# Performance work log

Measured on AMD Instinct MI355X. Metric: run time of the kernel, lower is better.

Reference implementation:

```python
import jax, jax.numpy as jnp
import numpy as np

# Contact model constants (from ContactModel defaults / hardcoded values)
STIFFNESS = 100000.0
DISSIPATION = 0.2
STATIC_FRICTION = 0.8
DYNAMIC_FRICTION = 0.8
VISCOUS_FRICTION = 0.5
TRANSITION_VELOCITY = 0.2
GROUND_HEIGHT = 0.0
DT = 0.05
RADIUS = 0.032
EPS = 1e-5
EPS2 = 1e-16
BV = 50.0
BD = 300.0

# 12 spheres: 6 right (bodies 4,5), 6 left (bodies 9,10)
SPHERE_BODY = np.array([4, 4, 4, 4, 5, 5, 9, 9, 9, 9, 10, 10], dtype=np.int32)
SPHERE_LOCAL = np.array([
    [0.00190115788407966, -0.01, -0.00382630379623308],
    [0.148386399942063,   -0.01, -0.028713422052654],
    [0.133001170607051,   -0.01,  0.0516362473449566],
    [0.0662346661991635,  -0.01,  0.0263641606741698],
    [0.06,                -0.01, -0.0187603084619177],
    [0.045,               -0.01,  0.0618569567549652],
    [0.00190115788407966, -0.01,  0.00382630379623308],
    [0.148386399942063,   -0.01,  0.028713422052654],
    [0.133001170607051,   -0.01, -0.0516362473449566],
    [0.0662346661991635,  -0.01, -0.0263641606741698],
    [0.06,                -0.01,  0.0187603084619177],
    [0.045,               -0.01, -0.0618569567549652],
], dtype=np.float32)
NORMAL = np.array([0.0, 1.0, 0.0], dtype=np.float32)


def _sphere_positions(joints, joints_ori):
    # joints: (B,24,3), joints_ori: (B,24,3,3) -> (B,12,3)
    body_pos = joints[:, SPHERE_BODY]            # (B,12,3)
    body_ori = joints_ori[:, SPHERE_BODY]        # (B,12,3,3)
    local = jnp.asarray(SPHERE_LOCAL)
    return body_pos + jnp.einsum('bsij,sj->bsi', body_ori, local)


def _contact_forces(pos, vel):
    # pos, vel: (B,S,3) -> forces (B,S,3); fully vectorized over spheres
    n = jnp.asarray(NORMAL)
    indentation = GROUND_HEIGHT - pos[..., 1]                    # (B,S)
    vnormal = vel[..., 1]                                        # dot(vel, [0,1,0])
    vtangent = vel - vnormal[..., None] * n                      # (B,S,3)
    ind_vel = -vnormal
    k = 0.5 * STIFFNESS ** (2.0 / 3.0)
    # sqrt(ind^2+eps)**1.5 == (ind^2+eps)**0.75
    fH = (4.0 / 3.0) * k * np.sqrt(RADIUS * k) * (indentation * indentation + EPS) ** 0.75
    fHd = fH * (1.0 + 1.5 * DISSIPATION * ind_vel)
    fn = ((0.5 * jnp.tanh(BV * (ind_vel + 1.0 / (1.5 * DISSIPATION))) + 0.5 + EPS2)
          * (0.5 * jnp.tanh(BD * indentation) + 0.5 + EPS2) * fHd)
    vslip = jnp.sqrt(jnp.sum(vtangent * vtangent, axis=-1) + EPS)
    vrel = vslip / TRANSITION_VELOCITY
    ffriction = fn * (jnp.minimum(vrel, 1.0)
                      * (DYNAMIC_FRICTION + 2.0 * (STATIC_FRICTION - DYNAMIC_FRICTION) / (1.0 + vrel * vrel))
                      + VISCOUS_FRICTION * vslip)
    force = fn[..., None] * n
    friction_force = ffriction[..., None] * (-vtangent) / (vslip[..., None] + EPS)
    return force + friction_force


def _cop_and_torque(pos, forces):
    # pos, forces: (B,S,3) -> cop (B,3), torque (B,3); vectorized batch version of the per-b loop
    vf = forces[..., 1]                          # (B,S)
    valid = vf > 0.0
    w = jnp.where(valid, vf, 0.0)
    tw = jnp.sum(w, axis=-1)                     # (B,)
    has = tw > 0.0
    tw_safe = jnp.where(has, tw, 1.0)
    cop_x = jnp.where(has, jnp.sum(pos[..., 0] * w, axis=-1) / tw_safe, 0.0)
    cop_y = jnp.where(has, GROUND_HEIGHT, 0.0)
    cop_z = jnp.where(has, jnp.sum(pos[..., 2] * w, axis=-1) / tw_safe, 0.0)
    cop = jnp.stack([cop_x, cop_y, cop_z], axis=-1)  # (B,3)
    r = pos - cop[:, None, :]
    f_masked = jnp.where(valid[..., None], forces, 0.0)  # only valid contacts contribute torque
    torque = jnp.sum(jnp.cross(r, f_masked), axis=1)
    return cop, torque


def setup_inputs() -> dict:
    key = jax.random.key(0)
    k1, k2 = jax.random.split(key)
    B = 262144
    joints = jax.random.normal(k1, (B, 24, 3), dtype=jnp.float32)
    joints_ori = jax.random.normal(k2, (B, 24, 3, 3), dtype=jnp.float32)
    return {"joints": joints, "joints_ori": joints_ori}


def reference(joints, joints_ori):
    pos = _sphere_positions(joints, joints_ori)              # (B,12,3)
    # finite-difference sphere velocity over frames (dt); zero at first frame
    vel = (pos - jnp.concatenate([pos[:1], pos[:-1]], axis=0)) / DT
    sphere_forces = _contact_forces(pos, vel)                # (B,12,3)

    force = jnp.sum(sphere_forces, axis=1)
    force_right = jnp.sum(sphere_forces[:, :6], axis=1)
    force_left = jnp.sum(sphere_forces[:, 6:], axis=1)
    cop, torque = _cop_and_torque(pos, sphere_forces)
    cop_right, torque_right = _cop_and_torque(pos[:, :6], sphere_forces[:, :6])
    cop_left, torque_left = _cop_and_torque(pos[:, 6:], sphere_forces[:, 6:])
    return (force, torque, cop, sphere_forces, pos,
            force_right, force_left, torque_right, torque_left, cop_right, cop_left)
```

## Files before the change

### kernel.cpp

```cpp
#include <hip/hip_runtime.h>
#include <math.h>


__device__ __constant__ float c_local[12][3] = {
    {0.00190115788407966f, -0.01f, -0.00382630379623308f},
    {0.148386399942063f,   -0.01f, -0.028713422052654f},
    {0.133001170607051f,   -0.01f,  0.0516362473449566f},
    {0.0662346661991635f,  -0.01f,  0.0263641606741698f},
    {0.06f,                -0.01f, -0.0187603084619177f},
    {0.045f,               -0.01f,  0.0618569567549652f},
    {0.00190115788407966f, -0.01f,  0.00382630379623308f},
    {0.148386399942063f,   -0.01f,  0.028713422052654f},
    {0.133001170607051f,   -0.01f, -0.0516362473449566f},
    {0.0662346661991635f,  -0.01f, -0.0263641606741698f},
    {0.06f,                -0.01f,  0.0187603084619177f},
    {0.045f,               -0.01f, -0.0618569567549652f}};

__global__ __launch_bounds__(256)
void contact_kernel(const float* __restrict__ joints,
                    const float* __restrict__ jori,
                    float* __restrict__ out, const int B)
{
    __shared__ float sbuf[256 * 37];
    const int tid = threadIdx.x;
    const int b = blockIdx.x * blockDim.x + tid;
    const bool full = ((B & 255) == 0);
    if (b >= B) return;

    float px[12], py[12], pz[12];
    float fx[12], fy[12], fz[12];

    {
        const int bodies[4] = {4, 5, 9, 10};
        const int sbeg[4]   = {0, 4, 6, 10};
        const int scnt[4]   = {4, 2, 4, 2};
        const int bp = (b > 0) ? (b - 1) : b;
        const float* jr  = joints + (size_t)b  * 72;
        const float* jrp = joints + (size_t)bp * 72;
        const float* mr  = jori   + (size_t)b  * 216;
        const float* mrp = jori   + (size_t)bp * 216;

        #pragma unroll
        for (int bi = 0; bi < 4; ++bi) {
            const int body = bodies[bi];
            const float jx = jr[body*3+0], jy = jr[body*3+1], jz = jr[body*3+2];
            const float* m = mr + body*9;
            const float m00=m[0],m01=m[1],m02=m[2];
            const float m10=m[3],m11=m[4],m12=m[5];
            const float m20=m[6],m21=m[7],m22=m[8];
            const float kx = jrp[body*3+0], ky = jrp[body*3+1], kz = jrp[body*3+2];
            const float* nn = mrp + body*9;
            const float n00=nn[0],n01=nn[1],n02=nn[2];
            const float n10=nn[3],n11=nn[4],n12=nn[5];
            const float n20=nn[6],n21=nn[7],n22=nn[8];
            #pragma unroll
            for (int si = 0; si < 4; ++si) {
                if (si < scnt[bi]) {
                    const int s = sbeg[bi] + si;
                    const float lx = c_local[s][0];
                    const float ly = c_local[s][1];
                    const float lz = c_local[s][2];
                    const float ax = jx + m00*lx + m01*ly + m02*lz;
                    const float ay = jy + m10*lx + m11*ly + m12*lz;
                    const float az = jz + m20*lx + m21*ly + m22*lz;
                    const float bx = kx + n00*lx + n01*ly + n02*lz;
                    const float by = ky + n10*lx + n11*ly + n12*lz;
                    const float bz = kz + n20*lx + n21*ly + n22*lz;
                    px[s] = ax; py[s] = ay; pz[s] = az;
                    fx[s] = (ax - bx) * 20.0f;
                    fy[s] = (ay - by) * 20.0f;
                    fz[s] = (az - bz) * 20.0f;
                }
            }
        }
    }

    const float KF  = 1077.21734501594f;
    const float CFH = (4.0f/3.0f) * KF * sqrtf(0.032f * KF);
    #pragma unroll
    for (int s = 0; s < 12; ++s) {
        const float vx = fx[s], vy = fy[s], vz = fz[s];
        const float ind     = -py[s];
        const float ind_vel = -vy;
        const float q   = ind*ind + 1e-5f;
        const float fH  = CFH * sqrtf(q * sqrtf(q));
        const float fHd = fH * (1.0f + 0.3f * ind_vel);
        const float t1 = (0.5f*tanhf(50.0f*(ind_vel + 3.3333333333333335f)) + 0.5f) + 1e-16f;
        const float t2 = (0.5f*tanhf(300.0f*ind) + 0.5f) + 1e-16f;
        const float fn = t1 * t2 * fHd;
        const float vslip = sqrtf(vx*vx + vz*vz + 1e-5f);
        const float vrel  = vslip * 5.0f;
        const float mu  = fminf(vrel, 1.0f) * 0.8f + 0.5f * vslip;
        const float ffr = fn * mu;
        const float sc  = ffr / (vslip + 1e-5f);
        fx[s] = -sc * vx;
        fy[s] = fn;
        fz[s] = -sc * vz;
    }

    float res[3][9];
    const int gs0[3] = {0, 0, 6};
    const int gs1[3] = {12, 6, 12};
    #pragma unroll
    for (int g = 0; g < 3; ++g) {
        float Fx=0.f, Fy=0.f, Fz=0.f, tw=0.f, sx=0.f, sz=0.f;
        #pragma unroll
        for (int s = 0; s < 12; ++s) {
            if (s >= gs0[g] && s < gs1[g]) {
                Fx += fx[s]; Fy += fy[s]; Fz += fz[s];
                const float w = fy[s] > 0.f ? fy[s] : 0.f;
                tw += w;
                sx += px[s] * w;
                sz += pz[s] * w;
            }
        }
        const bool has = tw > 0.f;
        const float cx = has ? sx / tw : 0.f;
        const float cz = has ? sz / tw : 0.f;
        float Tx=0.f, Ty=0.f, Tz=0.f;
        #pragma unroll
        for (int s = 0; s < 12; ++s) {
            if (s >= gs0[g] && s < gs1[g]) {
                if (fy[s] > 0.f) {
                    const float rx = px[s]-cx, ry = py[s], rz = pz[s]-cz;
                    Tx += ry*fz[s] - rz*fy[s];
                    Ty += rz*fx[s] - rx*fz[s];
                    Tz += rx*fy[s] - ry*fx[s];
                }
            }
        }
        res[g][0]=Fx; res[g][1]=Fy; res[g][2]=Fz;
        res[g][3]=Tx; res[g][4]=Ty; res[g][5]=Tz;
        res[g][6]=cx; res[g][7]=0.f; res[g][8]=cz;
    }

    const size_t sB = (size_t)B;
    const size_t t3 = (size_t)b * 3;
    float* o;
    o = out;           o[t3]=res[0][0]; o[t3+1]=res[0][1]; o[t3+2]=res[0][2];
    o = out + sB*3;    o[t3]=res[0][3]; o[t3+1]=res[0][4]; o[t3+2]=res[0][5];
    o = out + sB*6;    o[t3]=res[0][6]; o[t3+1]=res[0][7]; o[t3+2]=res[0][8];
    o = out + sB*81;   o[t3]=res[1][0]; o[t3+1]=res[1][1]; o[t3+2]=res[1][2];
    o = out + sB*84;   o[t3]=res[2][0]; o[t3+1]=res[2][1]; o[t3+2]=res[2][2];
    o = out + sB*87;   o[t3]=res[1][3]; o[t3+1]=res[1][4]; o[t3+2]=res[1][5];
    o = out + sB*90;   o[t3]=res[2][3]; o[t3+1]=res[2][4]; o[t3+2]=res[2][5];
    o = out + sB*93;   o[t3]=res[1][6]; o[t3+1]=res[1][7]; o[t3+2]=res[1][8];
    o = out + sB*96;   o[t3]=res[2][6]; o[t3+1]=res[2][7]; o[t3+2]=res[2][8];

    if (full) {
        #pragma unroll
        for (int s = 0; s < 12; ++s) {
            sbuf[tid*37 + s*3+0] = fx[s];
            sbuf[tid*37 + s*3+1] = fy[s];
            sbuf[tid*37 + s*3+2] = fz[s];
        }
        __syncthreads();
        {
            float4* dst = reinterpret_cast<float4*>(out + sB*9) + (size_t)blockIdx.x*2304;
            #pragma unroll
            for (int i = 0; i < 9; ++i) {
                const int j = tid + 256*i;
                const int g = 4*j;
                float v[4];
                #pragma unroll
                for (int e = 0; e < 4; ++e) {
                    const int gg = g+e; const int r = gg/36; const int c = gg-r*36;
                    v[e] = sbuf[r*37+c];
                }
                dst[j] = make_float4(v[0],v[1],v[2],v[3]);
            }
        }
        __syncthreads();
        #pragma unroll
        for (int s = 0; s < 12; ++s) {
            sbuf[tid*37 + s*3+0] = px[s];
            sbuf[tid*37 + s*3+1] = py[s];
            sbuf[tid*37 + s*3+2] = pz[s];
        }
        __syncthreads();
        {
            float4* dst = reinterpret_cast<float4*>(out + sB*45) + (size_t)blockIdx.x*2304;
            #pragma unroll
            for (int i = 0; i < 9; ++i) {
                const int j = tid + 256*i;
                const int g = 4*j;
                float v[4];
                #pragma unroll
                for (int e = 0; e < 4; ++e) {
                    const int gg = g+e; const int r = gg/36; const int c = gg-r*36;
                    v[e] = sbuf[r*37+c];
                }
                dst[j] = make_float4(v[0],v[1],v[2],v[3]);
            }
        }
    } else {
        float* osf = out + sB*9  + (size_t)b*36;
        float* opp = out + sB*45 + (size_t)b*36;
        #pragma unroll
        for (int s = 0; s < 12; ++s) {
            osf[s*3+0]=fx[s]; osf[s*3+1]=fy[s]; osf[s*3+2]=fz[s];
            opp[s*3+0]=px[s]; opp[s*3+1]=py[s]; opp[s*3+2]=pz[s];
        }
    }
}

extern "C" void kernel_launch(void* const* d_in, const int* in_sizes, int n_in,
                              void* d_out, int out_size, void* d_ws, size_t ws_size,
                              hipStream_t stream) {
    const float* joints = (const float*)d_in[0];
    const float* jori   = (const float*)d_in[1];
    float* out = (float*)d_out;
    const int B = in_sizes[0] / 72;
    const int block = 256;
    const int grid  = (B + block - 1) / block;
    contact_kernel<<<grid, block, 0, stream>>>(joints, jori, out, B);
}
```

Measured before the change: 63.47 us.

## Stage rotation matrices for block plus halo row through shared memory

```diff
diff --git a/kernel.cpp b/kernel.cpp
--- a/kernel.cpp
+++ b/kernel.cpp
@@ -21,34 +21,83 @@
                     const float* __restrict__ jori,
                     float* __restrict__ out, const int B)
 {
-    __shared__ float sbuf[256 * 37];
+    __shared__ float sbuf[257 * 37];
     const int tid = threadIdx.x;
     const int b = blockIdx.x * blockDim.x + tid;
     const bool full = ((B & 255) == 0);
-    if (b >= B) return;
 
     float px[12], py[12], pz[12];
     float fx[12], fy[12], fz[12];
 
-    {
+    const int bp = (b > 0) ? (b - 1) : b;
+    const float* jr  = joints + (size_t)b  * 72;
+    const float* jrp = joints + (size_t)bp * 72;
+
+    if (full) {
+        const long B0 = (long)blockIdx.x * 256;
+        for (int idx = tid; idx < 257 * 36; idx += 256) {
+            const int r = idx / 36, c = idx - r * 36;
+            long br = B0 - 1 + r;
+            br = br < 0 ? 0 : br;
+            const int off = (c < 18) ? (36 + c) : (63 + c);
+            sbuf[r * 37 + c] = jori[br * 216 + off];
+        }
+        __syncthreads();
+
+        const float* own = &sbuf[(tid + 1) * 37];
+        const float* prv = &sbuf[tid * 37];
         const int bodies[4] = {4, 5, 9, 10};
         const int sbeg[4]   = {0, 4, 6, 10};
         const int scnt[4]   = {4, 2, 4, 2};
-        const int bp = (b > 0) ? (b - 1) : b;
-        const float* jr  = joints + (size_t)b  * 72;
-        const float* jrp = joints + (size_t)bp * 72;
-        const float* mr  = jori   + (size_t)b  * 216;
-        const float* mrp = jori   + (size_t)bp * 216;
-
         #pragma unroll
         for (int bi = 0; bi < 4; ++bi) {
             const int body = bodies[bi];
             const float jx = jr[body*3+0], jy = jr[body*3+1], jz = jr[body*3+2];
+            const float kx = jrp[body*3+0], ky = jrp[body*3+1], kz = jrp[body*3+2];
+            const float* m  = own + bi*9;
+            const float m00=m[0],m01=m[1],m02=m[2];
+            const float m10=m[3],m11=m[4],m12=m[5];
+            const float m20=m[6],m21=m[7],m22=m[8];
+            const float* nn = prv + bi*9;
+            const float n00=nn[0],n01=nn[1],n02=nn[2];
+            const float n10=nn[3],n11=nn[4],n12=nn[5];
+            const float n20=nn[6],n21=nn[7],n22=nn[8];
+            #pragma unroll
+            for (int si = 0; si < 4; ++si) {
+                if (si < scnt[bi]) {
+                    const int s = sbeg[bi] + si;
+                    const float lx = c_local[s][0];
+                    const float ly = c_local[s][1];
+                    const float lz = c_local[s][2];
+                    const float ax = jx + m00*lx + m01*ly + m02*lz;
+                    const float ay = jy + m10*lx + m11*ly + m12*lz;
+                    const float az = jz + m20*lx + m21*ly + m22*lz;
+                    const float bx = kx + n00*lx + n01*ly + n02*lz;
+                    const float by = ky + n10*lx + n11*ly + n12*lz;
+                    const float bz = kz + n20*lx + n21*ly + n22*lz;
+                    px[s] = ax; py[s] = ay; pz[s] = az;
+                    fx[s] = (ax - bx) * 20.0f;
+                    fy[s] = (ay - by) * 20.0f;
+                    fz[s] = (az - bz) * 20.0f;
+                }
+            }
+        }
+    } else {
+        if (b >= B) return;
+        const float* mr  = jori + (size_t)b  * 216;
+        const float* mrp = jori + (size_t)bp * 216;
+        const int bodies[4] = {4, 5, 9, 10};
+        const int sbeg[4]   = {0, 4, 6, 10};
+        const int scnt[4]   = {4, 2, 4, 2};
+        #pragma unroll
+        for (int bi = 0; bi < 4; ++bi) {
+            const int body = bodies[bi];
+            const float jx = jr[body*3+0], jy = jr[body*3+1], jz = jr[body*3+2];
+            const float kx = jrp[body*3+0], ky = jrp[body*3+1], kz = jrp[body*3+2];
             const float* m = mr + body*9;
             const float m00=m[0],m01=m[1],m02=m[2];
             const float m10=m[3],m11=m[4],m12=m[5];
             const float m20=m[6],m21=m[7],m22=m[8];
-            const float kx = jrp[body*3+0], ky = jrp[body*3+1], kz = jrp[body*3+2];
             const float* nn = mrp + body*9;
             const float n00=nn[0],n01=nn[1],n02=nn[2];
             const float n10=nn[3],n11=nn[4],n12=nn[5];
@@ -148,6 +197,7 @@
     o = out + sB*96;   o[t3]=res[2][6]; o[t3+1]=res[2][7]; o[t3+2]=res[2][8];
 
     if (full) {
+        __syncthreads();
         #pragma unroll
         for (int s = 0; s < 12; ++s) {
             sbuf[tid*37 + s*3+0] = fx[s];
```

Measured after the change: 59.53 us (median of 2 runs). -6.2%, faster.
